# Kernel tuning notes

Measured on AMD Instinct MI355X. Metric: run time of the kernel, lower is better.

## Reference

```python
import jax, jax.numpy as jnp
import numpy as np

B, CIN, COUT, H, W, K = 4, 64, 64, 128, 128, 3
KK = K * K


def setup_inputs() -> dict:
    key = jax.random.key(0)
    k1, k2, k3, k4 = jax.random.split(key, 4)
    x = jax.random.normal(k1, (B, CIN, H, W), dtype=jnp.float32)
    offset = jax.random.normal(k2, (B, 2 * KK, H, W), dtype=jnp.float32)
    mask = jax.random.uniform(k3, (B, KK, H, W), dtype=jnp.float32)
    n = CIN * KK
    stdv = 1.0 / np.sqrt(n)
    weight = jax.random.uniform(k4, (COUT, CIN, K, K), dtype=jnp.float32,
                                minval=-stdv, maxval=stdv)
    bias = jnp.zeros((COUT,), dtype=jnp.float32)
    return {"x": x, "offset": offset, "mask": mask, "weight": weight, "bias": bias}


def _sample(x, ci, cj):
    # x: (b,c,h,w); ci,cj: (b,h,w,kk) int32 -> (b,c,h,w,kk), zero outside bounds
    b, c, h, w = x.shape
    valid = (ci >= 0) & (ci < h) & (cj >= 0) & (cj < w)  # (b,h,w,kk)
    idx = jnp.clip(ci, 0, h - 1) * w + jnp.clip(cj, 0, w - 1)
    flat = x.reshape(b, c, h * w)
    g = jnp.take_along_axis(flat, idx.reshape(b, 1, -1), axis=2)
    g = g.reshape(b, c, h, w, -1)
    return jnp.where(valid[:, None], g, jnp.zeros((), x.dtype))


def reference(x, offset, mask, weight, bias):
    b, c, h, w = x.shape
    # offset: (b, kk*2, h, w) -> (b, h, w, kk, 2)
    off = offset.reshape(b, KK, 2, h, w).transpose(0, 3, 4, 1, 2)
    # base sampling grid: coord[i,j,ki,kj] = (i-1+ki, j-1+kj), flattened over kk
    di, dj = jnp.meshgrid(jnp.arange(-(K // 2), K // 2 + 1),
                          jnp.arange(-(K // 2), K // 2 + 1), indexing='ij')
    base_i = jnp.arange(h, dtype=jnp.float32)[:, None, None] + di.reshape(1, 1, KK)
    base_j = jnp.arange(w, dtype=jnp.float32)[None, :, None] + dj.reshape(1, 1, KK)
    coord_i = off[..., 0] + base_i  # (b,h,w,kk)
    coord_j = off[..., 1] + base_j

    lt_i = jnp.floor(coord_i)
    lt_j = jnp.floor(coord_j)
    rb_i = jnp.ceil(coord_i)
    rb_j = jnp.ceil(coord_j)
    li, lj = lt_i.astype(jnp.int32), lt_j.astype(jnp.int32)
    ri, rj = rb_i.astype(jnp.int32), rb_j.astype(jnp.int32)

    v_lt = _sample(x, li, lj)
    v_rb = _sample(x, ri, rj)
    v_rt = _sample(x, li, rj)
    v_lb = _sample(x, ri, lj)

    # bilinear fractions, broadcast over channel dim
    fi = (coord_i - lt_i)[:, None]  # (b,1,h,w,kk)
    fj = (coord_j - lt_j)[:, None]
    v_t = v_lt + fj * (v_rt - v_lt)
    v_b = v_lb + fj * (v_rb - v_lb)
    v = v_t + fi * (v_b - v_t)  # (b,c,h,w,kk)

    # modulation mask: (b,kk,h,w) -> (b,1,h,w,kk)
    v = v * mask.transpose(0, 2, 3, 1)[:, None]

    w_flat = weight.reshape(weight.shape[0], c, KK)
    out = jnp.einsum('oik,bihwk->bohw', w_flat, v)
    return out + bias[None, :, None, None]
```

## Files before the change

kernel.cpp:

```cpp
#include <hip/hip_runtime.h>

#define B_   4
#define CIN  64
#define COUT 64
#define H_   128
#define W_   128
#define HW   (H_*W_)
#define KK   9
#define HALO 3
#define ROWS_R (8 + 2*HALO)
#define COLS_R (16 + 2*HALO)
#define RECS   (ROWS_R * COLS_R)
#define OFFB   (RECS * 128)
#define SMEMB  (OFFB + 27 * 128 * 4)
#define NBLK 512

typedef short bf16x8 __attribute__((ext_vector_type(8)));
typedef float f32x4  __attribute__((ext_vector_type(4)));
typedef float f32x2  __attribute__((ext_vector_type(2)));
typedef unsigned int u32;
typedef unsigned int u32x4 __attribute__((ext_vector_type(4)));

__device__ __forceinline__ unsigned short f2bf(float f) {
    unsigned int u = __float_as_uint(f);
    u = (u + 0x7FFFu + ((u >> 16) & 1u)) >> 16;
    return (unsigned short)u;
}

__global__ __launch_bounds__(256) void k_transpose(const float* __restrict__ x,
                                                   unsigned short* __restrict__ xt) {
    __shared__ float lds[64 * 129];
    int bi = blockIdx.x;
    int b = bi >> 7, i = bi & 127;
    int tid = threadIdx.x;
#pragma unroll
    for (int cc = 0; cc < 32; ++cc) {
        int c = cc * 2 + (tid >> 7);
        int w = tid & 127;
        lds[c * 129 + w] = x[((b * CIN + c) * H_ + i) * W_ + w];
    }
    __syncthreads();
#pragma unroll
    for (int q = 0; q < 32; ++q) {
        int c = tid & 63;
        int w = q * 4 + (tid >> 6);
        xt[((b * H_ + i) * W_ + w) * CIN + c] = f2bf(lds[c * 129 + w]);
    }
}

__global__ __launch_bounds__(256) void k_weight(const float* __restrict__ w,
                                                unsigned short* __restrict__ wtf) {
    int t = blockIdx.x * 256 + threadIdx.x;
    if (t >= 18 * 4 * 64 * 8) return;
    int j    = t & 7;
    int lane = (t >> 3) & 63;
    int nt   = (t >> 9) & 3;
    int s    = t >> 11;
    int kg   = s * 32 + ((lane >> 4) << 3) + j;
    int n    = nt * 16 + (lane & 15);
    int kpos = kg >> 6, c = kg & 63;
    wtf[t] = f2bf(w[(n * CIN + c) * 9 + kpos]);
}

__global__ __launch_bounds__(512, 6) void k_main(
    const unsigned short* __restrict__ xt,
    const float* __restrict__ offset,
    const float* __restrict__ mask,
    const unsigned short* __restrict__ wtf,
    const float* __restrict__ bias,
    float* __restrict__ out) {
    __shared__ __align__(16) unsigned char smem[SMEMB];

    const int tid  = threadIdx.x;
    const int lane = tid & 63;
    const int wv   = tid >> 6;
    const int T  = ((blockIdx.x & 7) << 6) + (blockIdx.x >> 3);
    const int b  = T >> 7;
    const int i0 = ((T >> 3) & 15) * 8;
    const int j0 = (T & 7) * 16;
    const char* xb = (const char*)xt + (size_t)b * HW * 128;

    {
        const int iA = i0 - HALO, jA = j0 - HALO;
#pragma unroll
        for (int k = 0; k < 5; ++k) {
            int idx = k * 512 + tid;
            if (idx < RECS * 8) {
                int rec = idx >> 3, c = idx & 7;
                int rr = rec / COLS_R, cc = rec - rr * COLS_R;
                int gr = min(max(iA + rr, 0), H_ - 1);
                int gc = min(max(jA + cc, 0), W_ - 1);
                u32x4 v = *(const u32x4*)(xb + (((gr << 7) + gc) << 7) + (c << 4));
                *(u32x4*)(smem + (rec << 7) + (((c + rec) & 7) << 4)) = v;
            }
        }
    }
    {
        const float* op = offset + (size_t)b * 18 * HW;
        const float* mp = mask   + (size_t)b * 9  * HW;
#pragma unroll
        for (int k = 0; k < 2; ++k) {
            int idx = k * 512 + tid;
            if (idx < 864) {
                int q = idx >> 5, rem = idx & 31;
                int row = rem >> 2, c4 = (rem & 3) << 2;
                const float* src = (q < 18 ? op + q * HW : mp + (q - 18) * HW)
                                   + (i0 + row) * W_ + j0 + c4;
                *(f32x4*)(smem + OFFB + idx * 16) = *(const f32x4*)src;
            }
        }
    }
    __syncthreads();

    const int p  = lane & 15;
    const int g  = lane >> 4;
    const int ir = i0 + wv;
    const int jc = j0 + p;
    const float* offl = (const float*)(smem + OFFB) + wv * 16 + p;
    const bf16x8* wp = (const bf16x8*)wtf;
    f32x4 acc0 = {0,0,0,0}, acc1 = {0,0,0,0}, acc2 = {0,0,0,0}, acc3 = {0,0,0,0};

#pragma unroll
    for (int kp = 0; kp < 9; ++kp) {
        float oi  = offl[(2 * kp) * 128];
        float oj  = offl[(2 * kp + 1) * 128];
        float msk = offl[(18 + kp) * 128];
        float ci = oi + (float)(ir + kp / 3 - 1);
        float cj = oj + (float)(jc + kp % 3 - 1);
        float fli = floorf(ci), flj = floorf(cj);
        float fi = ci - fli, fj = cj - flj;
        int li = (int)fli, lj = (int)flj;
        int li1 = li + 1, lj1 = lj + 1;
        float vy0 = (li  >= 0 && li  < H_) ? 1.f : 0.f;
        float vy1 = (li1 >= 0 && li1 < H_) ? 1.f : 0.f;
        float vx0 = (lj  >= 0 && lj  < W_) ? 1.f : 0.f;
        float vx1 = (lj1 >= 0 && lj1 < W_) ? 1.f : 0.f;
        float gi = fi * msk, gj = fj * msk;
        float w11 = gi * fj;
        f32x4 w4;
        w4.x = (msk - gi - gj + w11) * vy0 * vx0;
        w4.y = (gj - w11) * vy0 * vx1;
        w4.z = (gi - w11) * vy1 * vx0;
        w4.w = w11 * vy1 * vx1;
        int y0 = min(max(li,  0), H_ - 1), y1 = min(max(li1, 0), H_ - 1);
        int x0 = min(max(lj,  0), W_ - 1), x1 = min(max(lj1, 0), W_ - 1);
        int a00 = ((y0 << 7) + x0) << 7, a01 = ((y0 << 7) + x1) << 7;
        int a10 = ((y1 << 7) + x0) << 7, a11 = ((y1 << 7) + x1) << 7;
        int rli = li - (i0 - HALO), rlj = lj - (j0 - HALO);
        bool inr = ((unsigned)rli <= (unsigned)(ROWS_R - 2)) &&
                   ((unsigned)rlj <= (unsigned)(COLS_R - 2));
        int rli_c = min(max(rli, 0), ROWS_R - 2), rlj_c = min(max(rlj, 0), COLS_R - 2);
        int r00 = rli_c * COLS_R + rlj_c;
        int r01 = r00 + 1, r10 = r00 + COLS_R, r11 = r00 + COLS_R + 1;

        u32x4 q00[2], q01[2], q10[2], q11[2];
#pragma unroll
        for (int h = 0; h < 2; ++h) {
            int ch = h * 4 + g;
            q00[h] = *(const u32x4*)(smem + (r00 << 7) + (((ch + r00) & 7) << 4));
            q01[h] = *(const u32x4*)(smem + (r01 << 7) + (((ch + r01) & 7) << 4));
            q10[h] = *(const u32x4*)(smem + (r10 << 7) + (((ch + r10) & 7) << 4));
            q11[h] = *(const u32x4*)(smem + (r11 << 7) + (((ch + r11) & 7) << 4));
        }
        if (!inr) {
#pragma unroll
            for (int h = 0; h < 2; ++h) {
                int c = (g << 4) + (h << 6);
                q00[h] = *(const u32x4*)(xb + a00 + c);
                q01[h] = *(const u32x4*)(xb + a01 + c);
                q10[h] = *(const u32x4*)(xb + a10 + c);
                q11[h] = *(const u32x4*)(xb + a11 + c);
            }
        }
        f32x2 wx = {w4.x, w4.x}, wy = {w4.y, w4.y};
        f32x2 wz = {w4.z, w4.z}, ww = {w4.w, w4.w};
#pragma unroll
        for (int h = 0; h < 2; ++h) {
            u32x4 po;
#pragma unroll
            for (int q = 0; q < 4; ++q) {
                f32x2 c00 = {__uint_as_float(q00[h][q] << 16), __uint_as_float(q00[h][q] & 0xFFFF0000u)};
                f32x2 c01 = {__uint_as_float(q01[h][q] << 16), __uint_as_float(q01[h][q] & 0xFFFF0000u)};
                f32x2 c10 = {__uint_as_float(q10[h][q] << 16), __uint_as_float(q10[h][q] & 0xFFFF0000u)};
                f32x2 c11 = {__uint_as_float(q11[h][q] << 16), __uint_as_float(q11[h][q] & 0xFFFF0000u)};
                f32x2 r = wx * c00 + wy * c01 + wz * c10 + ww * c11;
                po[q] = __builtin_amdgcn_perm(__float_as_uint(r.y) + 0x8000u,
                                              __float_as_uint(r.x) + 0x8000u, 0x07060302u);
            }
            bf16x8 af; *(u32x4*)&af = po;
            int s = kp * 2 + h;
            acc0 = __builtin_amdgcn_mfma_f32_16x16x32_bf16(af, wp[(s*4+0)*64 + lane], acc0, 0, 0, 0);
            acc1 = __builtin_amdgcn_mfma_f32_16x16x32_bf16(af, wp[(s*4+1)*64 + lane], acc1, 0, 0, 0);
            acc2 = __builtin_amdgcn_mfma_f32_16x16x32_bf16(af, wp[(s*4+2)*64 + lane], acc2, 0, 0, 0);
            acc3 = __builtin_amdgcn_mfma_f32_16x16x32_bf16(af, wp[(s*4+3)*64 + lane], acc3, 0, 0, 0);
        }
    }

    __syncthreads();
    float* cst = (float*)smem;
    {
        f32x4 v0 = acc0, v1 = acc1, v2 = acc2, v3 = acc3;
        float bs0 = bias[p], bs1 = bias[16 + p], bs2 = bias[32 + p], bs3 = bias[48 + p];
#pragma unroll
        for (int r = 0; r < 4; ++r) { v0[r] += bs0; v1[r] += bs1; v2[r] += bs2; v3[r] += bs3; }
        const int pm = wv * 16 + (g << 2);
        *(f32x4*)&cst[(p)      * 132 + pm] = v0;
        *(f32x4*)&cst[(16 + p) * 132 + pm] = v1;
        *(f32x4*)&cst[(32 + p) * 132 + pm] = v2;
        *(f32x4*)&cst[(48 + p) * 132 + pm] = v3;
    }
    __syncthreads();
    const size_t obase = (size_t)b * (COUT * HW) + i0 * W_ + j0;
#pragma unroll
    for (int k = 0; k < 4; ++k) {
        int idx = k * 512 + tid;
        int cout = idx >> 5, chunk = idx & 31;
        int row = chunk >> 2, col = (chunk & 3) << 2;
        f32x4 vv = *(const f32x4*)&cst[cout * 132 + chunk * 4];
        __builtin_nontemporal_store(vv,
            (f32x4*)&out[obase + (size_t)cout * HW + row * W_ + col]);
    }
}

extern "C" void kernel_launch(void* const* d_in, const int* in_sizes, int n_in,
                              void* d_out, int out_size, void* d_ws, size_t ws_size,
                              hipStream_t stream) {
    const float* x      = (const float*)d_in[0];
    const float* offset = (const float*)d_in[1];
    const float* mask   = (const float*)d_in[2];
    const float* weight = (const float*)d_in[3];
    const float* bias   = (const float*)d_in[4];
    float* out = (float*)d_out;
    unsigned short* xt  = (unsigned short*)d_ws;
    unsigned short* wtf = xt + (size_t)B_ * H_ * W_ * CIN;

    k_transpose<<<B_ * H_, 256, 0, stream>>>(x, xt);
    k_weight<<<144, 256, 0, stream>>>(weight, wtf);
    k_main<<<NBLK, 512, 0, stream>>>(xt, offset, mask, wtf, bias, out);
}
```

Baseline: 35.57 us.

## Split kernel taps across wave halves and defer out-of-tile samples to fixup

```diff
diff --git a/kernel.cpp b/kernel.cpp
--- a/kernel.cpp
+++ b/kernel.cpp
@@ -8,12 +8,15 @@
 #define HW   (H_*W_)
 #define KK   9
 #define HALO 3
-#define ROWS_R (8 + 2*HALO)
-#define COLS_R (16 + 2*HALO)
+#define TI   4
+#define TJ   16
+#define ROWS_R (TI + 2*HALO)
+#define COLS_R (TJ + 2*HALO)
 #define RECS   (ROWS_R * COLS_R)
 #define OFFB   (RECS * 128)
-#define SMEMB  (OFFB + 27 * 128 * 4)
-#define NBLK 512
+#define SMEMB  (OFFB + 27 * TI * TJ * 4)
+#define NBLK   1024
+#define FCAP   16384
 
 typedef short bf16x8 __attribute__((ext_vector_type(8)));
 typedef float f32x4  __attribute__((ext_vector_type(4)));
@@ -25,6 +28,9 @@
     unsigned int u = __float_as_uint(f);
     u = (u + 0x7FFFu + ((u >> 16) & 1u)) >> 16;
     return (unsigned short)u;
+}
+__device__ __forceinline__ float bf2f(unsigned short s) {
+    return __uint_as_float(((unsigned int)s) << 16);
 }
 
 __global__ __launch_bounds__(256) void k_transpose(const float* __restrict__ x,
@@ -62,28 +68,39 @@
     wtf[t] = f2bf(w[(n * CIN + c) * 9 + kpos]);
 }
 
-__global__ __launch_bounds__(512, 6) void k_main(
+__global__ __launch_bounds__(256) void k_wfix(const float* __restrict__ w,
+                                              float* __restrict__ wfix) {
+    int t = blockIdx.x * 256 + threadIdx.x;
+    int kp = t >> 12, c = (t >> 6) & 63, cout = t & 63;
+    wfix[t] = w[(cout * CIN + c) * 9 + kp];
+}
+
+__global__ __launch_bounds__(512, 8) void k_main(
     const unsigned short* __restrict__ xt,
     const float* __restrict__ offset,
     const float* __restrict__ mask,
     const unsigned short* __restrict__ wtf,
     const float* __restrict__ bias,
-    float* __restrict__ out) {
+    float* __restrict__ out,
+    unsigned* __restrict__ counter,
+    unsigned* __restrict__ flags) {
     __shared__ __align__(16) unsigned char smem[SMEMB];
 
     const int tid  = threadIdx.x;
     const int lane = tid & 63;
     const int wv   = tid >> 6;
-    const int T  = ((blockIdx.x & 7) << 6) + (blockIdx.x >> 3);
-    const int b  = T >> 7;
-    const int i0 = ((T >> 3) & 15) * 8;
-    const int j0 = (T & 7) * 16;
+    const int wvl  = wv & 3;
+    const int half = wv >> 2;
+    const int T  = ((blockIdx.x & 7) << 7) + (blockIdx.x >> 3);
+    const int b  = T >> 8;
+    const int i0 = ((T >> 3) & 31) * TI;
+    const int j0 = (T & 7) * TJ;
     const char* xb = (const char*)xt + (size_t)b * HW * 128;
 
     {
         const int iA = i0 - HALO, jA = j0 - HALO;
 #pragma unroll
-        for (int k = 0; k < 5; ++k) {
+        for (int k = 0; k < 4; ++k) {
             int idx = k * 512 + tid;
             if (idx < RECS * 8) {
                 int rec = idx >> 3, c = idx & 7;
@@ -98,127 +115,186 @@
     {
         const float* op = offset + (size_t)b * 18 * HW;
         const float* mp = mask   + (size_t)b * 9  * HW;
-#pragma unroll
-        for (int k = 0; k < 2; ++k) {
-            int idx = k * 512 + tid;
-            if (idx < 864) {
-                int q = idx >> 5, rem = idx & 31;
-                int row = rem >> 2, c4 = (rem & 3) << 2;
-                const float* src = (q < 18 ? op + q * HW : mp + (q - 18) * HW)
-                                   + (i0 + row) * W_ + j0 + c4;
-                *(f32x4*)(smem + OFFB + idx * 16) = *(const f32x4*)src;
-            }
+        if (tid < 432) {
+            int q = tid >> 4, rem = tid & 15;
+            int row = rem >> 2, c4 = (rem & 3) << 2;
+            const float* src = (q < 18 ? op + q * HW : mp + (q - 18) * HW)
+                               + (i0 + row) * W_ + j0 + c4;
+            *(f32x4*)(smem + OFFB + tid * 16) = *(const f32x4*)src;
         }
     }
     __syncthreads();
 
     const int p  = lane & 15;
     const int g  = lane >> 4;
-    const int ir = i0 + wv;
+    const int ir = i0 + wvl;
     const int jc = j0 + p;
-    const float* offl = (const float*)(smem + OFFB) + wv * 16 + p;
+    const float* offl = (const float*)(smem + OFFB) + wvl * 16 + p;
     const bf16x8* wp = (const bf16x8*)wtf;
     f32x4 acc0 = {0,0,0,0}, acc1 = {0,0,0,0}, acc2 = {0,0,0,0}, acc3 = {0,0,0,0};
-
-#pragma unroll
-    for (int kp = 0; kp < 9; ++kp) {
-        float oi  = offl[(2 * kp) * 128];
-        float oj  = offl[(2 * kp + 1) * 128];
-        float msk = offl[(18 + kp) * 128];
-        float ci = oi + (float)(ir + kp / 3 - 1);
-        float cj = oj + (float)(jc + kp % 3 - 1);
+    int omask = 0;
+
+#define KP_BODY(KP, H0, H1, FLAG) do { \
+    float oi  = offl[(2*(KP)) * 64]; \
+    float oj  = offl[(2*(KP)+1) * 64]; \
+    float msk = offl[(18+(KP)) * 64]; \
+    float ci = oi + (float)(ir + (KP)/3 - 1); \
+    float cj = oj + (float)(jc + (KP)%3 - 1); \
+    float fli = floorf(ci), flj = floorf(cj); \
+    float fi = ci - fli, fj = cj - flj; \
+    int li = (int)fli, lj = (int)flj; \
+    int rli = li - (i0 - HALO), rlj = lj - (j0 - HALO); \
+    bool inr = ((unsigned)rli <= (unsigned)(ROWS_R-2)) && \
+               ((unsigned)rlj <= (unsigned)(COLS_R-2)); \
+    if (FLAG) omask |= (inr ? 0 : 1) << (KP); \
+    msk = inr ? msk : 0.f; \
+    float vy0 = (li   >= 0 && li   < H_) ? 1.f : 0.f; \
+    float vy1 = (li+1 >= 0 && li+1 < H_) ? 1.f : 0.f; \
+    float vx0 = (lj   >= 0 && lj   < W_) ? 1.f : 0.f; \
+    float vx1 = (lj+1 >= 0 && lj+1 < W_) ? 1.f : 0.f; \
+    float gi = fi * msk, gj = fj * msk; \
+    float w11 = gi * fj; \
+    float w4x = (msk - gi - gj + w11) * vy0 * vx0; \
+    float w4y = (gj - w11) * vy0 * vx1; \
+    float w4z = (gi - w11) * vy1 * vx0; \
+    float w4w = w11 * vy1 * vx1; \
+    int rli_c = min(max(rli, 0), ROWS_R-2), rlj_c = min(max(rlj, 0), COLS_R-2); \
+    int r00 = rli_c * COLS_R + rlj_c; \
+    int r01 = r00 + 1, r10 = r00 + COLS_R, r11 = r00 + COLS_R + 1; \
+    f32x2 wx = {w4x, w4x}, wy = {w4y, w4y}, wz = {w4z, w4z}, ww = {w4w, w4w}; \
+    _Pragma("unroll") \
+    for (int h = (H0); h < (H1); ++h) { \
+        int ch = h * 4 + g; \
+        u32x4 q00 = *(const u32x4*)(smem + (r00 << 7) + (((ch + r00) & 7) << 4)); \
+        u32x4 q01 = *(const u32x4*)(smem + (r01 << 7) + (((ch + r01) & 7) << 4)); \
+        u32x4 q10 = *(const u32x4*)(smem + (r10 << 7) + (((ch + r10) & 7) << 4)); \
+        u32x4 q11 = *(const u32x4*)(smem + (r11 << 7) + (((ch + r11) & 7) << 4)); \
+        u32x4 po; \
+        _Pragma("unroll") \
+        for (int q = 0; q < 4; ++q) { \
+            f32x2 c00 = {__uint_as_float(q00[q] << 16), __uint_as_float(q00[q] & 0xFFFF0000u)}; \
+            f32x2 c01 = {__uint_as_float(q01[q] << 16), __uint_as_float(q01[q] & 0xFFFF0000u)}; \
+            f32x2 c10 = {__uint_as_float(q10[q] << 16), __uint_as_float(q10[q] & 0xFFFF0000u)}; \
+            f32x2 c11 = {__uint_as_float(q11[q] << 16), __uint_as_float(q11[q] & 0xFFFF0000u)}; \
+            f32x2 r = wx * c00 + wy * c01 + wz * c10 + ww * c11; \
+            po[q] = __builtin_amdgcn_perm(__float_as_uint(r.y) + 0x8000u, \
+                                          __float_as_uint(r.x) + 0x8000u, 0x07060302u); \
+        } \
+        bf16x8 af; *(u32x4*)&af = po; \
+        int s = (KP) * 2 + h; \
+        acc0 = __builtin_amdgcn_mfma_f32_16x16x32_bf16(af, wp[(s*4+0)*64 + lane], acc0, 0, 0, 0); \
+        acc1 = __builtin_amdgcn_mfma_f32_16x16x32_bf16(af, wp[(s*4+1)*64 + lane], acc1, 0, 0, 0); \
+        acc2 = __builtin_amdgcn_mfma_f32_16x16x32_bf16(af, wp[(s*4+2)*64 + lane], acc2, 0, 0, 0); \
+        acc3 = __builtin_amdgcn_mfma_f32_16x16x32_bf16(af, wp[(s*4+3)*64 + lane], acc3, 0, 0, 0); \
+    } } while (0)
+
+    if (!half) {
+        KP_BODY(0, 0, 2, 1); KP_BODY(1, 0, 2, 1); KP_BODY(2, 0, 2, 1);
+        KP_BODY(3, 0, 2, 1); KP_BODY(8, 0, 1, 1);
+    } else {
+        KP_BODY(4, 0, 2, 1); KP_BODY(5, 0, 2, 1); KP_BODY(6, 0, 2, 1);
+        KP_BODY(7, 0, 2, 1); KP_BODY(8, 1, 2, 0);
+    }
+
+    if (g == 0 && omask) {
+        unsigned pxg = ((unsigned)b << 14) | ((unsigned)ir << 7) | (unsigned)jc;
+        while (omask) {
+            int kp = __ffs(omask) - 1; omask &= omask - 1;
+            unsigned idx = atomicAdd(counter, 1u);
+            if (idx < FCAP) flags[idx] = (pxg << 4) | (unsigned)kp;
+        }
+    }
+
+    __syncthreads();
+    f32x4* dump = (f32x4*)smem;
+    if (half) {
+        dump[(0*4 + wvl)*64 + lane] = acc0;
+        dump[(1*4 + wvl)*64 + lane] = acc1;
+        dump[(2*4 + wvl)*64 + lane] = acc2;
+        dump[(3*4 + wvl)*64 + lane] = acc3;
+    }
+    __syncthreads();
+    if (!half) {
+        acc0 += dump[(0*4 + wvl)*64 + lane];
+        acc1 += dump[(1*4 + wvl)*64 + lane];
+        acc2 += dump[(2*4 + wvl)*64 + lane];
+        acc3 += dump[(3*4 + wvl)*64 + lane];
+        float bs0 = bias[p], bs1 = bias[16 + p], bs2 = bias[32 + p], bs3 = bias[48 + p];
+#pragma unroll
+        for (int r = 0; r < 4; ++r) { acc0[r] += bs0; acc1[r] += bs1; acc2[r] += bs2; acc3[r] += bs3; }
+    }
+    __syncthreads();
+    float* cst = (float*)smem;
+    if (!half) {
+        const int pm = wvl * 16 + (g << 2);
+        *(f32x4*)&cst[(p)      * 68 + pm] = acc0;
+        *(f32x4*)&cst[(16 + p) * 68 + pm] = acc1;
+        *(f32x4*)&cst[(32 + p) * 68 + pm] = acc2;
+        *(f32x4*)&cst[(48 + p) * 68 + pm] = acc3;
+    }
+    __syncthreads();
+    const size_t obase = (size_t)b * (COUT * HW) + i0 * W_ + j0;
+#pragma unroll
+    for (int k = 0; k < 2; ++k) {
+        int idx = k * 512 + tid;
+        int cout = idx >> 4, chunk = idx & 15;
+        int row = chunk >> 2, cq = (chunk & 3) << 2;
+        f32x4 vv = *(const f32x4*)&cst[cout * 68 + chunk * 4];
+        __builtin_nontemporal_store(vv,
+            (f32x4*)&out[obase + (size_t)cout * HW + row * W_ + cq]);
+    }
+}
+
+__global__ __launch_bounds__(256) void k_fixup(
+    const unsigned short* __restrict__ xt,
+    const float* __restrict__ offset,
+    const float* __restrict__ mask,
+    const float* __restrict__ wfix,
+    const unsigned* __restrict__ counter,
+    const unsigned* __restrict__ flags,
+    float* __restrict__ out) {
+    const int wid  = (blockIdx.x * 256 + threadIdx.x) >> 6;
+    const int lane = threadIdx.x & 63;
+    unsigned n = *counter; if (n > FCAP) n = FCAP;
+    for (unsigned e = wid; e < n; e += 1024) {
+        unsigned code = flags[e];
+        int kp = code & 15;
+        unsigned px = code >> 4;
+        int b = px >> 14, ii = (px >> 7) & 127, jj = px & 127;
+        int hw = ii * W_ + jj;
+        float oi  = offset[((size_t)b * 18 + 2 * kp) * HW + hw];
+        float oj  = offset[((size_t)b * 18 + 2 * kp + 1) * HW + hw];
+        float msk = mask[((size_t)b * 9 + kp) * HW + hw];
+        int r3 = kp / 3;
+        float ci = oi + (float)(ii + r3 - 1);
+        float cj = oj + (float)(jj + (kp - r3 * 3) - 1);
         float fli = floorf(ci), flj = floorf(cj);
         float fi = ci - fli, fj = cj - flj;
         int li = (int)fli, lj = (int)flj;
-        int li1 = li + 1, lj1 = lj + 1;
-        float vy0 = (li  >= 0 && li  < H_) ? 1.f : 0.f;
-        float vy1 = (li1 >= 0 && li1 < H_) ? 1.f : 0.f;
-        float vx0 = (lj  >= 0 && lj  < W_) ? 1.f : 0.f;
-        float vx1 = (lj1 >= 0 && lj1 < W_) ? 1.f : 0.f;
+        float vy0 = (li   >= 0 && li   < H_) ? 1.f : 0.f;
+        float vy1 = (li+1 >= 0 && li+1 < H_) ? 1.f : 0.f;
+        float vx0 = (lj   >= 0 && lj   < W_) ? 1.f : 0.f;
+        float vx1 = (lj+1 >= 0 && lj+1 < W_) ? 1.f : 0.f;
+        int y0 = min(max(li,   0), H_ - 1), y1 = min(max(li+1, 0), H_ - 1);
+        int x0 = min(max(lj,   0), W_ - 1), x1 = min(max(lj+1, 0), W_ - 1);
         float gi = fi * msk, gj = fj * msk;
         float w11 = gi * fj;
-        f32x4 w4;
-        w4.x = (msk - gi - gj + w11) * vy0 * vx0;
-        w4.y = (gj - w11) * vy0 * vx1;
-        w4.z = (gi - w11) * vy1 * vx0;
-        w4.w = w11 * vy1 * vx1;
-        int y0 = min(max(li,  0), H_ - 1), y1 = min(max(li1, 0), H_ - 1);
-        int x0 = min(max(lj,  0), W_ - 1), x1 = min(max(lj1, 0), W_ - 1);
-        int a00 = ((y0 << 7) + x0) << 7, a01 = ((y0 << 7) + x1) << 7;
-        int a10 = ((y1 << 7) + x0) << 7, a11 = ((y1 << 7) + x1) << 7;
-        int rli = li - (i0 - HALO), rlj = lj - (j0 - HALO);
-        bool inr = ((unsigned)rli <= (unsigned)(ROWS_R - 2)) &&
-                   ((unsigned)rlj <= (unsigned)(COLS_R - 2));
-        int rli_c = min(max(rli, 0), ROWS_R - 2), rlj_c = min(max(rlj, 0), COLS_R - 2);
-        int r00 = rli_c * COLS_R + rlj_c;
-        int r01 = r00 + 1, r10 = r00 + COLS_R, r11 = r00 + COLS_R + 1;
-
-        u32x4 q00[2], q01[2], q10[2], q11[2];
-#pragma unroll
-        for (int h = 0; h < 2; ++h) {
-            int ch = h * 4 + g;
-            q00[h] = *(const u32x4*)(smem + (r00 << 7) + (((ch + r00) & 7) << 4));
-            q01[h] = *(const u32x4*)(smem + (r01 << 7) + (((ch + r01) & 7) << 4));
-            q10[h] = *(const u32x4*)(smem + (r10 << 7) + (((ch + r10) & 7) << 4));
-            q11[h] = *(const u32x4*)(smem + (r11 << 7) + (((ch + r11) & 7) << 4));
-        }
-        if (!inr) {
-#pragma unroll
-            for (int h = 0; h < 2; ++h) {
-                int c = (g << 4) + (h << 6);
-                q00[h] = *(const u32x4*)(xb + a00 + c);
-                q01[h] = *(const u32x4*)(xb + a01 + c);
-                q10[h] = *(const u32x4*)(xb + a10 + c);
-                q11[h] = *(const u32x4*)(xb + a11 + c);
-            }
-        }
-        f32x2 wx = {w4.x, w4.x}, wy = {w4.y, w4.y};
-        f32x2 wz = {w4.z, w4.z}, ww = {w4.w, w4.w};
-#pragma unroll
-        for (int h = 0; h < 2; ++h) {
-            u32x4 po;
-#pragma unroll
-            for (int q = 0; q < 4; ++q) {
-                f32x2 c00 = {__uint_as_float(q00[h][q] << 16), __uint_as_float(q00[h][q] & 0xFFFF0000u)};
-                f32x2 c01 = {__uint_as_float(q01[h][q] << 16), __uint_as_float(q01[h][q] & 0xFFFF0000u)};
-                f32x2 c10 = {__uint_as_float(q10[h][q] << 16), __uint_as_float(q10[h][q] & 0xFFFF0000u)};
-                f32x2 c11 = {__uint_as_float(q11[h][q] << 16), __uint_as_float(q11[h][q] & 0xFFFF0000u)};
-                f32x2 r = wx * c00 + wy * c01 + wz * c10 + ww * c11;
-                po[q] = __builtin_amdgcn_perm(__float_as_uint(r.y) + 0x8000u,
-                                              __float_as_uint(r.x) + 0x8000u, 0x07060302u);
-            }
-            bf16x8 af; *(u32x4*)&af = po;
-            int s = kp * 2 + h;
-            acc0 = __builtin_amdgcn_mfma_f32_16x16x32_bf16(af, wp[(s*4+0)*64 + lane], acc0, 0, 0, 0);
-            acc1 = __builtin_amdgcn_mfma_f32_16x16x32_bf16(af, wp[(s*4+1)*64 + lane], acc1, 0, 0, 0);
-            acc2 = __builtin_amdgcn_mfma_f32_16x16x32_bf16(af, wp[(s*4+2)*64 + lane], acc2, 0, 0, 0);
-            acc3 = __builtin_amdgcn_mfma_f32_16x16x32_bf16(af, wp[(s*4+3)*64 + lane], acc3, 0, 0, 0);
-        }
-    }
-
-    __syncthreads();
-    float* cst = (float*)smem;
-    {
-        f32x4 v0 = acc0, v1 = acc1, v2 = acc2, v3 = acc3;
-        float bs0 = bias[p], bs1 = bias[16 + p], bs2 = bias[32 + p], bs3 = bias[48 + p];
-#pragma unroll
-        for (int r = 0; r < 4; ++r) { v0[r] += bs0; v1[r] += bs1; v2[r] += bs2; v3[r] += bs3; }
-        const int pm = wv * 16 + (g << 2);
-        *(f32x4*)&cst[(p)      * 132 + pm] = v0;
-        *(f32x4*)&cst[(16 + p) * 132 + pm] = v1;
-        *(f32x4*)&cst[(32 + p) * 132 + pm] = v2;
-        *(f32x4*)&cst[(48 + p) * 132 + pm] = v3;
-    }
-    __syncthreads();
-    const size_t obase = (size_t)b * (COUT * HW) + i0 * W_ + j0;
-#pragma unroll
-    for (int k = 0; k < 4; ++k) {
-        int idx = k * 512 + tid;
-        int cout = idx >> 5, chunk = idx & 31;
-        int row = chunk >> 2, col = (chunk & 3) << 2;
-        f32x4 vv = *(const f32x4*)&cst[cout * 132 + chunk * 4];
-        __builtin_nontemporal_store(vv,
-            (f32x4*)&out[obase + (size_t)cout * HW + row * W_ + col]);
+        float w00 = (msk - gi - gj + w11) * vy0 * vx0;
+        float w01 = (gj - w11) * vy0 * vx1;
+        float w10 = (gi - w11) * vy1 * vx0;
+        float w11w = w11 * vy1 * vx1;
+        const unsigned short* xr = xt + (size_t)b * HW * CIN;
+        float v00 = bf2f(xr[((y0 << 7) + x0) * CIN + lane]);
+        float v01 = bf2f(xr[((y0 << 7) + x1) * CIN + lane]);
+        float v10 = bf2f(xr[((y1 << 7) + x0) * CIN + lane]);
+        float v11 = bf2f(xr[((y1 << 7) + x1) * CIN + lane]);
+        float v = w00 * v00 + w01 * v01 + w10 * v10 + w11w * v11;
+        float acc = 0.f;
+        const float* wk = wfix + (size_t)kp * 64 * 64 + lane;
+#pragma unroll 8
+        for (int c = 0; c < 64; ++c)
+            acc = fmaf(__shfl(v, c), wk[c * 64], acc);
+        atomicAdd(&out[((size_t)(b * COUT) + lane) * HW + hw], acc);
     }
 }
 
@@ -231,10 +307,17 @@
     const float* weight = (const float*)d_in[3];
     const float* bias   = (const float*)d_in[4];
     float* out = (float*)d_out;
-    unsigned short* xt  = (unsigned short*)d_ws;
-    unsigned short* wtf = xt + (size_t)B_ * H_ * W_ * CIN;
-
+    char* ws = (char*)d_ws;
+    unsigned short* xt  = (unsigned short*)ws;
+    unsigned short* wtf = (unsigned short*)(ws + 8388608);
+    float* wfix         = (float*)(ws + 8388608 + 73728);
+    unsigned* counter   = (unsigned*)(ws + 8388608 + 73728 + 147456);
+    unsigned* flags     = counter + 32;
+
+    hipMemsetAsync(counter, 0, 4, stream);
     k_transpose<<<B_ * H_, 256, 0, stream>>>(x, xt);
     k_weight<<<144, 256, 0, stream>>>(weight, wtf);
-    k_main<<<NBLK, 512, 0, stream>>>(xt, offset, mask, wtf, bias, out);
-}
+    k_wfix<<<144, 256, 0, stream>>>(weight, wfix);
+    k_main<<<NBLK, 512, 0, stream>>>(xt, offset, mask, wtf, bias, out, counter, flags);
+    k_fixup<<<256, 256, 0, stream>>>(xt, offset, mask, wfix, counter, flags, out);
+}
```

After: 93.57 us. 163% more time.

## Double-buffer weight fragment loads via inline asm and preload offsets to registers

Applied to the files above, without the earlier changes.

```diff
diff --git a/kernel.cpp b/kernel.cpp
--- a/kernel.cpp
+++ b/kernel.cpp
@@ -62,7 +62,7 @@
     wtf[t] = f2bf(w[(n * CIN + c) * 9 + kpos]);
 }
 
-__global__ __launch_bounds__(512, 6) void k_main(
+__global__ __launch_bounds__(512, 4) void k_main(
     const unsigned short* __restrict__ xt,
     const float* __restrict__ offset,
     const float* __restrict__ mask,
@@ -79,6 +79,20 @@
     const int i0 = ((T >> 3) & 15) * 8;
     const int j0 = (T & 7) * 16;
     const char* xb = (const char*)xt + (size_t)b * HW * 128;
+    const char* bbase = (const char*)wtf + (size_t)lane * 16;
+
+    bf16x8 bA0, bA1, bA2, bA3, bB0, bB1, bB2, bB3;
+#define ISSUE_B(S, B0, B1, B2, B3) do { \
+    const char* _ba = bbase + (S) * 4096; \
+    asm volatile( \
+        "global_load_dwordx4 %0, %4, off\n\t" \
+        "global_load_dwordx4 %1, %4, off offset:1024\n\t" \
+        "global_load_dwordx4 %2, %4, off offset:2048\n\t" \
+        "global_load_dwordx4 %3, %4, off offset:3072" \
+        : "=&v"(B0), "=&v"(B1), "=&v"(B2), "=&v"(B3) \
+        : "v"(_ba) : "memory"); \
+} while (0)
+    ISSUE_B(0, bA0, bA1, bA2, bA3);
 
     {
         const int iA = i0 - HALO, jA = j0 - HALO;
@@ -117,82 +131,95 @@
     const int ir = i0 + wv;
     const int jc = j0 + p;
     const float* offl = (const float*)(smem + OFFB) + wv * 16 + p;
-    const bf16x8* wp = (const bf16x8*)wtf;
+    float offv[18], mskv[9];
+#pragma unroll
+    for (int q = 0; q < 18; ++q) offv[q] = offl[q * 128];
+#pragma unroll
+    for (int q = 0; q < 9; ++q)  mskv[q] = offl[(18 + q) * 128];
+
     f32x4 acc0 = {0,0,0,0}, acc1 = {0,0,0,0}, acc2 = {0,0,0,0}, acc3 = {0,0,0,0};
 
+#define BLEND(AF) do { \
+    u32x4 po; \
+    _Pragma("unroll") \
+    for (int q = 0; q < 4; ++q) { \
+        f32x2 c00 = {__uint_as_float(q00[q] << 16), __uint_as_float(q00[q] & 0xFFFF0000u)}; \
+        f32x2 c01 = {__uint_as_float(q01[q] << 16), __uint_as_float(q01[q] & 0xFFFF0000u)}; \
+        f32x2 c10 = {__uint_as_float(q10[q] << 16), __uint_as_float(q10[q] & 0xFFFF0000u)}; \
+        f32x2 c11 = {__uint_as_float(q11[q] << 16), __uint_as_float(q11[q] & 0xFFFF0000u)}; \
+        f32x2 r = wx * c00 + wy * c01 + wz * c10 + ww * c11; \
+        po[q] = __builtin_amdgcn_perm(__float_as_uint(r.y) + 0x8000u, \
+                                      __float_as_uint(r.x) + 0x8000u, 0x07060302u); \
+    } \
+    *(u32x4*)&(AF) = po; } while (0)
+
+#define CORNERS(H) \
+    int ch = (H) * 4 + g; \
+    u32x4 q00 = *(const u32x4*)(smem + (r00 << 7) + (((ch + r00) & 7) << 4)); \
+    u32x4 q01 = *(const u32x4*)(smem + (r01 << 7) + (((ch + r01) & 7) << 4)); \
+    u32x4 q10 = *(const u32x4*)(smem + (r10 << 7) + (((ch + r10) & 7) << 4)); \
+    u32x4 q11 = *(const u32x4*)(smem + (r11 << 7) + (((ch + r11) & 7) << 4)); \
+    if (!inr) { \
+        int c = (g << 4) + ((H) << 6); \
+        q00 = *(const u32x4*)(xb + a00 + c); \
+        q01 = *(const u32x4*)(xb + a01 + c); \
+        q10 = *(const u32x4*)(xb + a10 + c); \
+        q11 = *(const u32x4*)(xb + a11 + c); \
+    }
+
+#define WAIT_MFMA(AF, B0, B1, B2, B3) do { \
+    asm volatile("s_waitcnt vmcnt(0)" ::: "memory"); \
+    __builtin_amdgcn_sched_barrier(0); \
+    acc0 = __builtin_amdgcn_mfma_f32_16x16x32_bf16(AF, B0, acc0, 0, 0, 0); \
+    acc1 = __builtin_amdgcn_mfma_f32_16x16x32_bf16(AF, B1, acc1, 0, 0, 0); \
+    acc2 = __builtin_amdgcn_mfma_f32_16x16x32_bf16(AF, B2, acc2, 0, 0, 0); \
+    acc3 = __builtin_amdgcn_mfma_f32_16x16x32_bf16(AF, B3, acc3, 0, 0, 0); } while (0)
+
 #pragma unroll
     for (int kp = 0; kp < 9; ++kp) {
-        float oi  = offl[(2 * kp) * 128];
-        float oj  = offl[(2 * kp + 1) * 128];
-        float msk = offl[(18 + kp) * 128];
+        float oi  = offv[2 * kp];
+        float oj  = offv[2 * kp + 1];
+        float msk = mskv[kp];
         float ci = oi + (float)(ir + kp / 3 - 1);
         float cj = oj + (float)(jc + kp % 3 - 1);
         float fli = floorf(ci), flj = floorf(cj);
         float fi = ci - fli, fj = cj - flj;
         int li = (int)fli, lj = (int)flj;
-        int li1 = li + 1, lj1 = lj + 1;
-        float vy0 = (li  >= 0 && li  < H_) ? 1.f : 0.f;
-        float vy1 = (li1 >= 0 && li1 < H_) ? 1.f : 0.f;
-        float vx0 = (lj  >= 0 && lj  < W_) ? 1.f : 0.f;
-        float vx1 = (lj1 >= 0 && lj1 < W_) ? 1.f : 0.f;
-        float gi = fi * msk, gj = fj * msk;
-        float w11 = gi * fj;
-        f32x4 w4;
-        w4.x = (msk - gi - gj + w11) * vy0 * vx0;
-        w4.y = (gj - w11) * vy0 * vx1;
-        w4.z = (gi - w11) * vy1 * vx0;
-        w4.w = w11 * vy1 * vx1;
-        int y0 = min(max(li,  0), H_ - 1), y1 = min(max(li1, 0), H_ - 1);
-        int x0 = min(max(lj,  0), W_ - 1), x1 = min(max(lj1, 0), W_ - 1);
-        int a00 = ((y0 << 7) + x0) << 7, a01 = ((y0 << 7) + x1) << 7;
-        int a10 = ((y1 << 7) + x0) << 7, a11 = ((y1 << 7) + x1) << 7;
         int rli = li - (i0 - HALO), rlj = lj - (j0 - HALO);
         bool inr = ((unsigned)rli <= (unsigned)(ROWS_R - 2)) &&
                    ((unsigned)rlj <= (unsigned)(COLS_R - 2));
+        float vy0 = (li   >= 0 && li   < H_) ? 1.f : 0.f;
+        float vy1 = (li+1 >= 0 && li+1 < H_) ? 1.f : 0.f;
+        float vx0 = (lj   >= 0 && lj   < W_) ? 1.f : 0.f;
+        float vx1 = (lj+1 >= 0 && lj+1 < W_) ? 1.f : 0.f;
+        float gi = fi * msk, gj = fj * msk;
+        float w11 = gi * fj;
+        float w4x = (msk - gi - gj + w11) * vy0 * vx0;
+        float w4y = (gj - w11) * vy0 * vx1;
+        float w4z = (gi - w11) * vy1 * vx0;
+        float w4w = w11 * vy1 * vx1;
+        f32x2 wx = {w4x, w4x}, wy = {w4y, w4y}, wz = {w4z, w4z}, ww = {w4w, w4w};
+        int y0 = min(max(li,   0), H_ - 1), y1 = min(max(li+1, 0), H_ - 1);
+        int x0 = min(max(lj,   0), W_ - 1), x1 = min(max(lj+1, 0), W_ - 1);
+        int a00 = ((y0 << 7) + x0) << 7, a01 = ((y0 << 7) + x1) << 7;
+        int a10 = ((y1 << 7) + x0) << 7, a11 = ((y1 << 7) + x1) << 7;
         int rli_c = min(max(rli, 0), ROWS_R - 2), rlj_c = min(max(rlj, 0), COLS_R - 2);
         int r00 = rli_c * COLS_R + rlj_c;
         int r01 = r00 + 1, r10 = r00 + COLS_R, r11 = r00 + COLS_R + 1;
 
-        u32x4 q00[2], q01[2], q10[2], q11[2];
-#pragma unroll
-        for (int h = 0; h < 2; ++h) {
-            int ch = h * 4 + g;
-            q00[h] = *(const u32x4*)(smem + (r00 << 7) + (((ch + r00) & 7) << 4));
-            q01[h] = *(const u32x4*)(smem + (r01 << 7) + (((ch + r01) & 7) << 4));
-            q10[h] = *(const u32x4*)(smem + (r10 << 7) + (((ch + r10) & 7) << 4));
-            q11[h] = *(const u32x4*)(smem + (r11 << 7) + (((ch + r11) & 7) << 4));
-        }
-        if (!inr) {
-#pragma unroll
-            for (int h = 0; h < 2; ++h) {
-                int c = (g << 4) + (h << 6);
-                q00[h] = *(const u32x4*)(xb + a00 + c);
-                q01[h] = *(const u32x4*)(xb + a01 + c);
-                q10[h] = *(const u32x4*)(xb + a10 + c);
-                q11[h] = *(const u32x4*)(xb + a11 + c);
-            }
-        }
-        f32x2 wx = {w4.x, w4.x}, wy = {w4.y, w4.y};
-        f32x2 wz = {w4.z, w4.z}, ww = {w4.w, w4.w};
-#pragma unroll
-        for (int h = 0; h < 2; ++h) {
-            u32x4 po;
-#pragma unroll
-            for (int q = 0; q < 4; ++q) {
-                f32x2 c00 = {__uint_as_float(q00[h][q] << 16), __uint_as_float(q00[h][q] & 0xFFFF0000u)};
-                f32x2 c01 = {__uint_as_float(q01[h][q] << 16), __uint_as_float(q01[h][q] & 0xFFFF0000u)};
-                f32x2 c10 = {__uint_as_float(q10[h][q] << 16), __uint_as_float(q10[h][q] & 0xFFFF0000u)};
-                f32x2 c11 = {__uint_as_float(q11[h][q] << 16), __uint_as_float(q11[h][q] & 0xFFFF0000u)};
-                f32x2 r = wx * c00 + wy * c01 + wz * c10 + ww * c11;
-                po[q] = __builtin_amdgcn_perm(__float_as_uint(r.y) + 0x8000u,
-                                              __float_as_uint(r.x) + 0x8000u, 0x07060302u);
-            }
-            bf16x8 af; *(u32x4*)&af = po;
-            int s = kp * 2 + h;
-            acc0 = __builtin_amdgcn_mfma_f32_16x16x32_bf16(af, wp[(s*4+0)*64 + lane], acc0, 0, 0, 0);
-            acc1 = __builtin_amdgcn_mfma_f32_16x16x32_bf16(af, wp[(s*4+1)*64 + lane], acc1, 0, 0, 0);
-            acc2 = __builtin_amdgcn_mfma_f32_16x16x32_bf16(af, wp[(s*4+2)*64 + lane], acc2, 0, 0, 0);
-            acc3 = __builtin_amdgcn_mfma_f32_16x16x32_bf16(af, wp[(s*4+3)*64 + lane], acc3, 0, 0, 0);
+        {
+            ISSUE_B(2 * kp + 1, bB0, bB1, bB2, bB3);
+            CORNERS(0);
+            bf16x8 af;
+            BLEND(af);
+            WAIT_MFMA(af, bA0, bA1, bA2, bA3);
+        }
+        {
+            if (kp < 8) ISSUE_B(2 * kp + 2, bA0, bA1, bA2, bA3);
+            CORNERS(1);
+            bf16x8 af;
+            BLEND(af);
+            WAIT_MFMA(af, bB0, bB1, bB2, bB3);
         }
     }
 
@@ -231,8 +258,9 @@
     const float* weight = (const float*)d_in[3];
     const float* bias   = (const float*)d_in[4];
     float* out = (float*)d_out;
-    unsigned short* xt  = (unsigned short*)d_ws;
-    unsigned short* wtf = xt + (size_t)B_ * H_ * W_ * CIN;
+    char* ws = (char*)d_ws;
+    unsigned short* xt  = (unsigned short*)ws;
+    unsigned short* wtf = (unsigned short*)(ws + 8388608);
 
     k_transpose<<<B_ * H_, 256, 0, stream>>>(x, xt);
     k_weight<<<144, 256, 0, stream>>>(weight, wtf);
```

Result: slower. 39.74 us (+11.7%).

## Split deformable sampling into LDS-only fast pass and wave-uniform global fallback pass

Applied to the files above, without the earlier changes.

```diff
diff --git a/kernel.cpp b/kernel.cpp
--- a/kernel.cpp
+++ b/kernel.cpp
@@ -119,80 +119,90 @@
     const float* offl = (const float*)(smem + OFFB) + wv * 16 + p;
     const bf16x8* wp = (const bf16x8*)wtf;
     f32x4 acc0 = {0,0,0,0}, acc1 = {0,0,0,0}, acc2 = {0,0,0,0}, acc3 = {0,0,0,0};
+    int emask = 0;
+
+#define KP_META(KP, OUTP) \
+    float oi  = offl[(2*(KP)) * 128]; \
+    float oj  = offl[(2*(KP)+1) * 128]; \
+    float msk = offl[(18+(KP)) * 128]; \
+    float ci = oi + (float)(ir + (KP)/3 - 1); \
+    float cj = oj + (float)(jc + (KP)%3 - 1); \
+    float fli = floorf(ci), flj = floorf(cj); \
+    float fi = ci - fli, fj = cj - flj; \
+    int li = (int)fli, lj = (int)flj; \
+    int rli = li - (i0 - HALO), rlj = lj - (j0 - HALO); \
+    bool inr = ((unsigned)rli <= (unsigned)(ROWS_R - 2)) && \
+               ((unsigned)rlj <= (unsigned)(COLS_R - 2)); \
+    msk = (inr != (bool)(OUTP)) ? msk : 0.f; \
+    float vy0 = (li   >= 0 && li   < H_) ? 1.f : 0.f; \
+    float vy1 = (li+1 >= 0 && li+1 < H_) ? 1.f : 0.f; \
+    float vx0 = (lj   >= 0 && lj   < W_) ? 1.f : 0.f; \
+    float vx1 = (lj+1 >= 0 && lj+1 < W_) ? 1.f : 0.f; \
+    float gi = fi * msk, gj = fj * msk; \
+    float w11 = gi * fj; \
+    float w4x = (msk - gi - gj + w11) * vy0 * vx0; \
+    float w4y = (gj - w11) * vy0 * vx1; \
+    float w4z = (gi - w11) * vy1 * vx0; \
+    float w4w = w11 * vy1 * vx1; \
+    f32x2 wx = {w4x, w4x}, wy = {w4y, w4y}, wz = {w4z, w4z}, ww = {w4w, w4w};
+
+#define BLEND_MFMA(S) do { \
+    u32x4 po; \
+    _Pragma("unroll") \
+    for (int q = 0; q < 4; ++q) { \
+        f32x2 c00 = {__uint_as_float(q00[q] << 16), __uint_as_float(q00[q] & 0xFFFF0000u)}; \
+        f32x2 c01 = {__uint_as_float(q01[q] << 16), __uint_as_float(q01[q] & 0xFFFF0000u)}; \
+        f32x2 c10 = {__uint_as_float(q10[q] << 16), __uint_as_float(q10[q] & 0xFFFF0000u)}; \
+        f32x2 c11 = {__uint_as_float(q11[q] << 16), __uint_as_float(q11[q] & 0xFFFF0000u)}; \
+        f32x2 r = wx * c00 + wy * c01 + wz * c10 + ww * c11; \
+        po[q] = __builtin_amdgcn_perm(__float_as_uint(r.y) + 0x8000u, \
+                                      __float_as_uint(r.x) + 0x8000u, 0x07060302u); \
+    } \
+    bf16x8 af; *(u32x4*)&af = po; \
+    acc0 = __builtin_amdgcn_mfma_f32_16x16x32_bf16(af, wp[((S)*4+0)*64 + lane], acc0, 0, 0, 0); \
+    acc1 = __builtin_amdgcn_mfma_f32_16x16x32_bf16(af, wp[((S)*4+1)*64 + lane], acc1, 0, 0, 0); \
+    acc2 = __builtin_amdgcn_mfma_f32_16x16x32_bf16(af, wp[((S)*4+2)*64 + lane], acc2, 0, 0, 0); \
+    acc3 = __builtin_amdgcn_mfma_f32_16x16x32_bf16(af, wp[((S)*4+3)*64 + lane], acc3, 0, 0, 0); } while (0)
 
 #pragma unroll
     for (int kp = 0; kp < 9; ++kp) {
-        float oi  = offl[(2 * kp) * 128];
-        float oj  = offl[(2 * kp + 1) * 128];
-        float msk = offl[(18 + kp) * 128];
-        float ci = oi + (float)(ir + kp / 3 - 1);
-        float cj = oj + (float)(jc + kp % 3 - 1);
-        float fli = floorf(ci), flj = floorf(cj);
-        float fi = ci - fli, fj = cj - flj;
-        int li = (int)fli, lj = (int)flj;
-        int li1 = li + 1, lj1 = lj + 1;
-        float vy0 = (li  >= 0 && li  < H_) ? 1.f : 0.f;
-        float vy1 = (li1 >= 0 && li1 < H_) ? 1.f : 0.f;
-        float vx0 = (lj  >= 0 && lj  < W_) ? 1.f : 0.f;
-        float vx1 = (lj1 >= 0 && lj1 < W_) ? 1.f : 0.f;
-        float gi = fi * msk, gj = fj * msk;
-        float w11 = gi * fj;
-        f32x4 w4;
-        w4.x = (msk - gi - gj + w11) * vy0 * vx0;
-        w4.y = (gj - w11) * vy0 * vx1;
-        w4.z = (gi - w11) * vy1 * vx0;
-        w4.w = w11 * vy1 * vx1;
-        int y0 = min(max(li,  0), H_ - 1), y1 = min(max(li1, 0), H_ - 1);
-        int x0 = min(max(lj,  0), W_ - 1), x1 = min(max(lj1, 0), W_ - 1);
-        int a00 = ((y0 << 7) + x0) << 7, a01 = ((y0 << 7) + x1) << 7;
-        int a10 = ((y1 << 7) + x0) << 7, a11 = ((y1 << 7) + x1) << 7;
-        int rli = li - (i0 - HALO), rlj = lj - (j0 - HALO);
-        bool inr = ((unsigned)rli <= (unsigned)(ROWS_R - 2)) &&
-                   ((unsigned)rlj <= (unsigned)(COLS_R - 2));
+        KP_META(kp, 0);
+        if (__any(!inr)) emask |= 1 << kp;
         int rli_c = min(max(rli, 0), ROWS_R - 2), rlj_c = min(max(rlj, 0), COLS_R - 2);
         int r00 = rli_c * COLS_R + rlj_c;
         int r01 = r00 + 1, r10 = r00 + COLS_R, r11 = r00 + COLS_R + 1;
-
-        u32x4 q00[2], q01[2], q10[2], q11[2];
 #pragma unroll
         for (int h = 0; h < 2; ++h) {
             int ch = h * 4 + g;
-            q00[h] = *(const u32x4*)(smem + (r00 << 7) + (((ch + r00) & 7) << 4));
-            q01[h] = *(const u32x4*)(smem + (r01 << 7) + (((ch + r01) & 7) << 4));
-            q10[h] = *(const u32x4*)(smem + (r10 << 7) + (((ch + r10) & 7) << 4));
-            q11[h] = *(const u32x4*)(smem + (r11 << 7) + (((ch + r11) & 7) << 4));
-        }
-        if (!inr) {
+            u32x4 q00 = *(const u32x4*)(smem + (r00 << 7) + (((ch + r00) & 7) << 4));
+            u32x4 q01 = *(const u32x4*)(smem + (r01 << 7) + (((ch + r01) & 7) << 4));
+            u32x4 q10 = *(const u32x4*)(smem + (r10 << 7) + (((ch + r10) & 7) << 4));
+            u32x4 q11 = *(const u32x4*)(smem + (r11 << 7) + (((ch + r11) & 7) << 4));
+            BLEND_MFMA(kp * 2 + h);
+        }
+    }
+
+#pragma unroll
+    for (int kp = 0; kp < 9; ++kp) {
+        if (emask & (1 << kp)) {
+            KP_META(kp, 1);
+            int y0 = min(max(li,   0), H_ - 1), y1 = min(max(li+1, 0), H_ - 1);
+            int x0 = min(max(lj,   0), W_ - 1), x1 = min(max(lj+1, 0), W_ - 1);
+            int a00 = ((y0 << 7) + x0) << 7, a01 = ((y0 << 7) + x1) << 7;
+            int a10 = ((y1 << 7) + x0) << 7, a11 = ((y1 << 7) + x1) << 7;
 #pragma unroll
             for (int h = 0; h < 2; ++h) {
                 int c = (g << 4) + (h << 6);
-                q00[h] = *(const u32x4*)(xb + a00 + c);
-                q01[h] = *(const u32x4*)(xb + a01 + c);
-                q10[h] = *(const u32x4*)(xb + a10 + c);
-                q11[h] = *(const u32x4*)(xb + a11 + c);
+                u32x4 z = {0u, 0u, 0u, 0u};
+                u32x4 q00 = z, q01 = z, q10 = z, q11 = z;
+                if (!inr) {
+                    q00 = *(const u32x4*)(xb + a00 + c);
+                    q01 = *(const u32x4*)(xb + a01 + c);
+                    q10 = *(const u32x4*)(xb + a10 + c);
+                    q11 = *(const u32x4*)(xb + a11 + c);
+                }
+                BLEND_MFMA(kp * 2 + h);
             }
-        }
-        f32x2 wx = {w4.x, w4.x}, wy = {w4.y, w4.y};
-        f32x2 wz = {w4.z, w4.z}, ww = {w4.w, w4.w};
-#pragma unroll
-        for (int h = 0; h < 2; ++h) {
-            u32x4 po;
-#pragma unroll
-            for (int q = 0; q < 4; ++q) {
-                f32x2 c00 = {__uint_as_float(q00[h][q] << 16), __uint_as_float(q00[h][q] & 0xFFFF0000u)};
-                f32x2 c01 = {__uint_as_float(q01[h][q] << 16), __uint_as_float(q01[h][q] & 0xFFFF0000u)};
-                f32x2 c10 = {__uint_as_float(q10[h][q] << 16), __uint_as_float(q10[h][q] & 0xFFFF0000u)};
-                f32x2 c11 = {__uint_as_float(q11[h][q] << 16), __uint_as_float(q11[h][q] & 0xFFFF0000u)};
-                f32x2 r = wx * c00 + wy * c01 + wz * c10 + ww * c11;
-                po[q] = __builtin_amdgcn_perm(__float_as_uint(r.y) + 0x8000u,
-                                              __float_as_uint(r.x) + 0x8000u, 0x07060302u);
-            }
-            bf16x8 af; *(u32x4*)&af = po;
-            int s = kp * 2 + h;
-            acc0 = __builtin_amdgcn_mfma_f32_16x16x32_bf16(af, wp[(s*4+0)*64 + lane], acc0, 0, 0, 0);
-            acc1 = __builtin_amdgcn_mfma_f32_16x16x32_bf16(af, wp[(s*4+1)*64 + lane], acc1, 0, 0, 0);
-            acc2 = __builtin_amdgcn_mfma_f32_16x16x32_bf16(af, wp[(s*4+2)*64 + lane], acc2, 0, 0, 0);
-            acc3 = __builtin_amdgcn_mfma_f32_16x16x32_bf16(af, wp[(s*4+3)*64 + lane], acc3, 0, 0, 0);
         }
     }
 
@@ -231,8 +241,9 @@
     const float* weight = (const float*)d_in[3];
     const float* bias   = (const float*)d_in[4];
     float* out = (float*)d_out;
-    unsigned short* xt  = (unsigned short*)d_ws;
-    unsigned short* wtf = xt + (size_t)B_ * H_ * W_ * CIN;
+    char* ws = (char*)d_ws;
+    unsigned short* xt  = (unsigned short*)ws;
+    unsigned short* wtf = (unsigned short*)(ws + 8388608);
 
     k_transpose<<<B_ * H_, 256, 0, stream>>>(x, xt);
     k_weight<<<144, 256, 0, stream>>>(weight, wtf);
```

Result: slower. 75.82 us (+113.2%).
